# Performance work log

Hardware: AMD Instinct MI355X
Metric: run time of the kernel (lower is better)

The kernel has to match this reference:

```python
import jax, jax.numpy as jnp
import numpy as np

NU, NV = 8192, 8192
IN_DIM, HID, NCLS = 128, 64, 5


def setup_inputs() -> dict:
    key = jax.random.key(0)
    k1, k2, k3, k4, k5, k6, k7 = jax.random.split(key, 7)
    return {
        "u": jax.random.normal(k1, (NU, IN_DIM), dtype=jnp.float32),
        "v": jax.random.normal(k2, (NV, IN_DIM), dtype=jnp.float32),
        "adj": jax.random.uniform(k3, (NU, NV), dtype=jnp.float32),
        "degree": jax.random.uniform(k4, (NU + NV,), dtype=jnp.float32),
        "u_weight": jax.random.normal(k5, (NCLS, IN_DIM, HID), dtype=jnp.float32),
        "v_weight": jax.random.normal(k6, (NCLS, IN_DIM, HID), dtype=jnp.float32),
        "bias": jax.random.normal(k7, (HID,), dtype=jnp.float32),
        "r": 4,
    }


def reference(u, v, adj, degree, u_weight, v_weight, bias, r):
    # Sum weight slices for rating classes 0..r (r is a static Python int).
    Wu = jnp.sum(u_weight[: r + 1], axis=0)  # [IN_DIM, HID]
    Wv = jnp.sum(v_weight[: r + 1], axis=0)
    # Dropout is identity at p=0.0 (eval mode).
    su = u @ Wu  # [NU, HID]
    sv = v @ Wv  # [NV, HID]
    nu = adj.shape[0]
    # Block adjacency [[0, A], [A^T, 0]] row-scaled by diag(degree), applied to
    # concat(su, sv) -- computed block-wise, same math without the dense block matrix.
    top = degree[:nu, None] * (adj @ sv)      # [NU, HID]
    bot = degree[nu:, None] * (adj.T @ su)    # [NV, HID]
    return jnp.concatenate([top, bot], axis=0) + bias
```

## Files before the change

kernel.cpp:

```cpp
#include <hip/hip_runtime.h>
#include <stdint.h>


#define HID 64
#define IN_DIM 128
#define NROWS 8192
#define NCLS 5

typedef float f32x4 __attribute__((ext_vector_type(4)));
typedef short s16x8 __attribute__((ext_vector_type(8)));
typedef unsigned short u16;

static __device__ __forceinline__ short f2b(float x) {
    unsigned u = __builtin_bit_cast(unsigned, x);
    return (short)((u + 0x7FFFu + ((u >> 16) & 1u)) >> 16);
}

static __device__ __forceinline__ void cp16(const void* g, void* l) {
    __builtin_amdgcn_global_load_lds(
        (const __attribute__((address_space(1))) void*)g,
        (__attribute__((address_space(3))) void*)l, 16, 0, 0);
}

__global__ __launch_bounds__(256, 2) void k_prep(
    const float* __restrict__ u, const float* __restrict__ v,
    const float* __restrict__ uw, const float* __restrict__ vw,
    const int* __restrict__ rp, u16* __restrict__ ws)
{
    __shared__ float W[IN_DIM * HID];
    __shared__ float X[64 * 129];

    const int y = blockIdx.y;
    const float* __restrict__ src  = y ? v  : u;
    const float* __restrict__ wsrc = y ? vw : uw;
    u16* __restrict__ dstT = ws + (size_t)y * (HID * NROWS);
    const int i0 = blockIdx.x * 64;
    const int t = threadIdx.x;
    int r = *rp; if (r > NCLS - 1) r = NCLS - 1; if (r < 0) r = 0;

    for (int idx = t; idx < IN_DIM * HID; idx += 256) {
        float s = 0.f;
        for (int c = 0; c <= r; ++c) s += wsrc[c * (IN_DIM * HID) + idx];
        W[idx] = s;
    }
    #pragma unroll
    for (int qq = 0; qq < 8; ++qq) {
        int idx = t + qq * 256;
        int row = idx >> 5, c4 = idx & 31;
        f32x4 val = *(const f32x4*)&src[(size_t)(i0 + row) * IN_DIM + c4 * 4];
        float* d = &X[row * 129 + c4 * 4];
        d[0] = val[0]; d[1] = val[1]; d[2] = val[2]; d[3] = val[3];
    }
    __syncthreads();

    const int i = t & 63, h0 = (t >> 6) * 16;
    float acc[16];
    #pragma unroll
    for (int k = 0; k < 16; ++k) acc[k] = 0.f;
    for (int c = 0; c < IN_DIM; ++c) {
        float uv = X[i * 129 + c];
        const f32x4* wr = (const f32x4*)&W[c * HID + h0];
        f32x4 w0 = wr[0], w1 = wr[1], w2 = wr[2], w3 = wr[3];
        acc[0]  += uv * w0[0]; acc[1]  += uv * w0[1];
        acc[2]  += uv * w0[2]; acc[3]  += uv * w0[3];
        acc[4]  += uv * w1[0]; acc[5]  += uv * w1[1];
        acc[6]  += uv * w1[2]; acc[7]  += uv * w1[3];
        acc[8]  += uv * w2[0]; acc[9]  += uv * w2[1];
        acc[10] += uv * w2[2]; acc[11] += uv * w2[3];
        acc[12] += uv * w3[0]; acc[13] += uv * w3[1];
        acc[14] += uv * w3[2]; acc[15] += uv * w3[3];
    }
    #pragma unroll
    for (int hh = 0; hh < 16; ++hh)
        dstT[(size_t)(h0 + hh) * NROWS + i0 + i] = (u16)f2b(acc[hh]);
}

__global__ __launch_bounds__(256, 2) void k_main(
    const float* __restrict__ adj, const float* __restrict__ degree,
    const float* __restrict__ bias, const u16* __restrict__ ws,
    float* __restrict__ out)
{
    __shared__ float At[2][2048];
    __shared__ u16   Bt[2][4096];

    const int mode = blockIdx.y;
    const int bx = blockIdx.x;
    const int t = threadIdx.x;
    const int w = t >> 6, l = t & 63;
    const int q = l >> 4, l15 = l & 15;
    const int mt = w & 1;
    const int nh = w >> 1;
    const int m0 = bx * 32;
    const u16* __restrict__ BT = ws + (mode == 0 ? (size_t)(HID * NROWS) : 0);

    f32x4 acc[2];
    acc[0] = (f32x4){0.f, 0.f, 0.f, 0.f};
    acc[1] = (f32x4){0.f, 0.f, 0.f, 0.f};

    auto stage = [&](int step, int buf) {
        int kc = (mode == 0) ? (((bx >> 1) + step) & 127)
                             : (((bx >> 1) - step) & 127);
        int k0 = kc * 64;
        if (mode == 0) {
            #pragma unroll
            for (int t2 = 0; t2 < 2; ++t2) {
                int s = w * 2 + t2;
                int row = s * 4 + (l >> 4);
                int cg = (l & 15) ^ (row & 15);
                cp16(&adj[(size_t)(m0 + row) * NROWS + k0 + cg * 4],
                     &At[buf][s * 256]);
            }
        } else {
            #pragma unroll
            for (int t2 = 0; t2 < 2; ++t2) {
                int s = w * 2 + t2;
                int row = s * 8 + (l >> 3);
                int cg = (l & 7) ^ (row & 7);
                cp16(&adj[(size_t)(k0 + row) * NROWS + m0 + cg * 4],
                     &At[buf][s * 256]);
            }
        }
        #pragma unroll
        for (int t2 = 0; t2 < 2; ++t2) {
            int s = w * 2 + t2;
            int n = s * 8 + (l >> 3);
            int cg = (l & 7) ^ (n & 7);
            cp16(&BT[(size_t)n * NROWS + k0 + cg * 8], &Bt[buf][s * 512]);
        }
    };

    stage(0, 0);
    __syncthreads();
    int buf = 0;
    for (int step = 0; step < 128; ++step) {
        if (step < 127) stage(step + 1, buf ^ 1);
        const float* __restrict__ A = At[buf];
        const u16* __restrict__ B = Bt[buf];
        #pragma unroll
        for (int kh = 0; kh < 2; ++kh) {
            s16x8 af;
            if (mode == 0) {
                const int ii = mt * 16 + l15;
                const int cgk = kh * 8 + q * 2;
                f32x4 f0 = *(const f32x4*)&A[ii * 64 + ((cgk    ) ^ (ii & 15)) * 4];
                f32x4 f1 = *(const f32x4*)&A[ii * 64 + ((cgk + 1) ^ (ii & 15)) * 4];
                af[0] = f2b(f0[0]); af[1] = f2b(f0[1]);
                af[2] = f2b(f0[2]); af[3] = f2b(f0[3]);
                af[4] = f2b(f1[0]); af[5] = f2b(f1[1]);
                af[6] = f2b(f1[2]); af[7] = f2b(f1[3]);
            } else {
                const int jj = mt * 16 + l15;
                const int cg = jj >> 2, jr = jj & 3;
                #pragma unroll
                for (int tt = 0; tt < 8; ++tt) {
                    int ii = kh * 32 + q * 8 + tt;
                    af[tt] = f2b(A[ii * 32 + ((cg ^ (ii & 7)) << 2) + jr]);
                }
            }
            #pragma unroll
            for (int nn = 0; nn < 2; ++nn) {
                int n = (nh * 2 + nn) * 16 + l15;
                int cgl = (kh * 4 + q) ^ (n & 7);
                s16x8 bf = *(const s16x8*)&B[n * 64 + cgl * 8];
                acc[nn] = __builtin_amdgcn_mfma_f32_16x16x32_bf16(af, bf, acc[nn], 0, 0, 0);
            }
        }
        __syncthreads();
        buf ^= 1;
    }

    const int obase = (mode == 0) ? 0 : NROWS;
    const float* __restrict__ degp = degree + obase;
    #pragma unroll
    for (int nn = 0; nn < 2; ++nn) {
        int n = (nh * 2 + nn) * 16 + l15;
        float bs = bias[n];
        #pragma unroll
        for (int rg = 0; rg < 4; ++rg) {
            int m = m0 + mt * 16 + q * 4 + rg;
            out[(size_t)(obase + m) * HID + n] = degp[m] * acc[nn][rg] + bs;
        }
    }
}

extern "C" void kernel_launch(void* const* d_in, const int* in_sizes, int n_in,
                              void* d_out, int out_size, void* d_ws, size_t ws_size,
                              hipStream_t stream) {
    (void)in_sizes; (void)n_in; (void)out_size; (void)ws_size;
    const float* u      = (const float*)d_in[0];
    const float* v      = (const float*)d_in[1];
    const float* adj    = (const float*)d_in[2];
    const float* degree = (const float*)d_in[3];
    const float* uw     = (const float*)d_in[4];
    const float* vw     = (const float*)d_in[5];
    const float* bias   = (const float*)d_in[6];
    const int*   rp     = (const int*)d_in[7];
    u16*   ws  = (u16*)d_ws;
    float* out = (float*)d_out;

    k_prep<<<dim3(128, 2), 256, 0, stream>>>(u, v, uw, vw, rp, ws);
    k_main<<<dim3(256, 2), 256, 0, stream>>>(adj, degree, bias, ws, out);
}
```

Baseline: 493.3 us.

## Split K across waves with direct global loads and LDS reduction

Restructures k_main so each of the four waves owns a quarter of the K range and computes the full 32x64 output tile, rather than splitting the M/N tile across waves. The block-shared double-buffered global_load_lds staging and per-step __syncthreads are dropped. Mode 0 now loads adj and B fragments straight from global memory into registers. Mode 1 transposes through a per-wave padded LDS tile, and the four partial accumulators are summed in LDS at the end before vectorized stores. This removes block-wide barriers and lets waves run independently, at the cost of more registers, less sharing of B loads between waves, and uncoalesced direct global fragment loads.

```diff
diff --git a/kernel.cpp b/kernel.cpp
--- a/kernel.cpp
+++ b/kernel.cpp
@@ -14,12 +14,6 @@
 static __device__ __forceinline__ short f2b(float x) {
     unsigned u = __builtin_bit_cast(unsigned, x);
     return (short)((u + 0x7FFFu + ((u >> 16) & 1u)) >> 16);
-}
-
-static __device__ __forceinline__ void cp16(const void* g, void* l) {
-    __builtin_amdgcn_global_load_lds(
-        (const __attribute__((address_space(1))) void*)g,
-        (__attribute__((address_space(3))) void*)l, 16, 0, 0);
 }
 
 __global__ __launch_bounds__(256, 2) void k_prep(
@@ -80,107 +74,123 @@
     const float* __restrict__ bias, const u16* __restrict__ ws,
     float* __restrict__ out)
 {
-    __shared__ float At[2][2048];
-    __shared__ u16   Bt[2][4096];
+    __shared__ float S[4][64 * 33];
 
     const int mode = blockIdx.y;
     const int bx = blockIdx.x;
     const int t = threadIdx.x;
     const int w = t >> 6, l = t & 63;
     const int q = l >> 4, l15 = l & 15;
-    const int mt = w & 1;
-    const int nh = w >> 1;
     const int m0 = bx * 32;
+    const unsigned a = (unsigned)(bx >> 1);
+    const int kbase = w * 2048;
     const u16* __restrict__ BT = ws + (mode == 0 ? (size_t)(HID * NROWS) : 0);
 
-    f32x4 acc[2];
-    acc[0] = (f32x4){0.f, 0.f, 0.f, 0.f};
-    acc[1] = (f32x4){0.f, 0.f, 0.f, 0.f};
-
-    auto stage = [&](int step, int buf) {
-        int kc = (mode == 0) ? (((bx >> 1) + step) & 127)
-                             : (((bx >> 1) - step) & 127);
-        int k0 = kc * 64;
-        if (mode == 0) {
-            #pragma unroll
-            for (int t2 = 0; t2 < 2; ++t2) {
-                int s = w * 2 + t2;
-                int row = s * 4 + (l >> 4);
-                int cg = (l & 15) ^ (row & 15);
-                cp16(&adj[(size_t)(m0 + row) * NROWS + k0 + cg * 4],
-                     &At[buf][s * 256]);
-            }
-        } else {
-            #pragma unroll
-            for (int t2 = 0; t2 < 2; ++t2) {
-                int s = w * 2 + t2;
-                int row = s * 8 + (l >> 3);
-                int cg = (l & 7) ^ (row & 7);
-                cp16(&adj[(size_t)(k0 + row) * NROWS + m0 + cg * 4],
-                     &At[buf][s * 256]);
+    f32x4 acc[2][4];
+    #pragma unroll
+    for (int i = 0; i < 2; ++i)
+        #pragma unroll
+        for (int j = 0; j < 4; ++j) acc[i][j] = (f32x4){0.f, 0.f, 0.f, 0.f};
+
+    if (mode == 0) {
+        const float* __restrict__ ap0 = adj + (size_t)(m0 + l15) * NROWS;
+        const float* __restrict__ ap1 = ap0 + (size_t)16 * NROWS;
+        for (int tau = 0; tau < 32; ++tau) {
+            const int k0 = kbase + (int)(((a + tau) & 31u) << 6);
+            #pragma unroll
+            for (int kh = 0; kh < 2; ++kh) {
+                const int k = k0 + kh * 32 + q * 8;
+                f32x4 a00 = *(const f32x4*)(ap0 + k);
+                f32x4 a01 = *(const f32x4*)(ap0 + k + 4);
+                f32x4 a10 = *(const f32x4*)(ap1 + k);
+                f32x4 a11 = *(const f32x4*)(ap1 + k + 4);
+                s16x8 bf[4];
+                #pragma unroll
+                for (int nn = 0; nn < 4; ++nn)
+                    bf[nn] = *(const s16x8*)(BT + (size_t)(nn * 16 + l15) * NROWS + k);
+                s16x8 af0, af1;
+                af0[0]=f2b(a00[0]); af0[1]=f2b(a00[1]); af0[2]=f2b(a00[2]); af0[3]=f2b(a00[3]);
+                af0[4]=f2b(a01[0]); af0[5]=f2b(a01[1]); af0[6]=f2b(a01[2]); af0[7]=f2b(a01[3]);
+                af1[0]=f2b(a10[0]); af1[1]=f2b(a10[1]); af1[2]=f2b(a10[2]); af1[3]=f2b(a10[3]);
+                af1[4]=f2b(a11[0]); af1[5]=f2b(a11[1]); af1[6]=f2b(a11[2]); af1[7]=f2b(a11[3]);
+                #pragma unroll
+                for (int nn = 0; nn < 4; ++nn) {
+                    acc[0][nn] = __builtin_amdgcn_mfma_f32_16x16x32_bf16(af0, bf[nn], acc[0][nn], 0, 0, 0);
+                    acc[1][nn] = __builtin_amdgcn_mfma_f32_16x16x32_bf16(af1, bf[nn], acc[1][nn], 0, 0, 0);
+                }
             }
         }
-        #pragma unroll
-        for (int t2 = 0; t2 < 2; ++t2) {
-            int s = w * 2 + t2;
-            int n = s * 8 + (l >> 3);
-            int cg = (l & 7) ^ (n & 7);
-            cp16(&BT[(size_t)n * NROWS + k0 + cg * 8], &Bt[buf][s * 512]);
-        }
-    };
-
-    stage(0, 0);
-    __syncthreads();
-    int buf = 0;
-    for (int step = 0; step < 128; ++step) {
-        if (step < 127) stage(step + 1, buf ^ 1);
-        const float* __restrict__ A = At[buf];
-        const u16* __restrict__ B = Bt[buf];
-        #pragma unroll
-        for (int kh = 0; kh < 2; ++kh) {
-            s16x8 af;
-            if (mode == 0) {
-                const int ii = mt * 16 + l15;
-                const int cgk = kh * 8 + q * 2;
-                f32x4 f0 = *(const f32x4*)&A[ii * 64 + ((cgk    ) ^ (ii & 15)) * 4];
-                f32x4 f1 = *(const f32x4*)&A[ii * 64 + ((cgk + 1) ^ (ii & 15)) * 4];
-                af[0] = f2b(f0[0]); af[1] = f2b(f0[1]);
-                af[2] = f2b(f0[2]); af[3] = f2b(f0[3]);
-                af[4] = f2b(f1[0]); af[5] = f2b(f1[1]);
-                af[6] = f2b(f1[2]); af[7] = f2b(f1[3]);
-            } else {
-                const int jj = mt * 16 + l15;
-                const int cg = jj >> 2, jr = jj & 3;
-                #pragma unroll
-                for (int tt = 0; tt < 8; ++tt) {
-                    int ii = kh * 32 + q * 8 + tt;
-                    af[tt] = f2b(A[ii * 32 + ((cg ^ (ii & 7)) << 2) + jr]);
+    } else {
+        float* __restrict__ T = S[w];
+        const int wr_r = l >> 3;
+        const int wr_c = (l & 7) * 4;
+        const float* __restrict__ cb = adj + m0 + wr_c;
+        for (int tau = 0; tau < 32; ++tau) {
+            const int i0 = kbase + (int)(((a - tau) & 31u) << 6);
+            f32x4 tr[8];
+            #pragma unroll
+            for (int c = 0; c < 8; ++c)
+                tr[c] = *(const f32x4*)(cb + (size_t)(i0 + c * 8 + wr_r) * NROWS);
+            #pragma unroll
+            for (int c = 0; c < 8; ++c) {
+                float* d = &T[(c * 8 + wr_r) * 33 + wr_c];
+                d[0] = tr[c][0]; d[1] = tr[c][1]; d[2] = tr[c][2]; d[3] = tr[c][3];
+            }
+            asm volatile("s_waitcnt lgkmcnt(0)" ::: "memory");
+            #pragma unroll
+            for (int kh = 0; kh < 2; ++kh) {
+                const int kk = i0 + kh * 32 + q * 8;
+                s16x8 bf[4];
+                #pragma unroll
+                for (int nn = 0; nn < 4; ++nn)
+                    bf[nn] = *(const s16x8*)(BT + (size_t)(nn * 16 + l15) * NROWS + kk);
+                s16x8 af[2];
+                #pragma unroll
+                for (int mt = 0; mt < 2; ++mt) {
+                    const int j = mt * 16 + l15;
+                    #pragma unroll
+                    for (int tt = 0; tt < 8; ++tt)
+                        af[mt][tt] = f2b(T[(kh * 32 + q * 8 + tt) * 33 + j]);
+                }
+                #pragma unroll
+                for (int nn = 0; nn < 4; ++nn) {
+                    acc[0][nn] = __builtin_amdgcn_mfma_f32_16x16x32_bf16(af[0], bf[nn], acc[0][nn], 0, 0, 0);
+                    acc[1][nn] = __builtin_amdgcn_mfma_f32_16x16x32_bf16(af[1], bf[nn], acc[1][nn], 0, 0, 0);
                 }
             }
-            #pragma unroll
-            for (int nn = 0; nn < 2; ++nn) {
-                int n = (nh * 2 + nn) * 16 + l15;
-                int cgl = (kh * 4 + q) ^ (n & 7);
-                s16x8 bf = *(const s16x8*)&B[n * 64 + cgl * 8];
-                acc[nn] = __builtin_amdgcn_mfma_f32_16x16x32_bf16(af, bf, acc[nn], 0, 0, 0);
-            }
+            asm volatile("" ::: "memory");
         }
-        __syncthreads();
-        buf ^= 1;
-    }
-
-    const int obase = (mode == 0) ? 0 : NROWS;
-    const float* __restrict__ degp = degree + obase;
-    #pragma unroll
-    for (int nn = 0; nn < 2; ++nn) {
-        int n = (nh * 2 + nn) * 16 + l15;
-        float bs = bias[n];
+    }
+
+    asm volatile("" ::: "memory");
+    {
+        float* __restrict__ P = S[w];
         #pragma unroll
-        for (int rg = 0; rg < 4; ++rg) {
-            int m = m0 + mt * 16 + q * 4 + rg;
-            out[(size_t)(obase + m) * HID + n] = degp[m] * acc[nn][rg] + bs;
-        }
-    }
+        for (int mt = 0; mt < 2; ++mt)
+            #pragma unroll
+            for (int nn = 0; nn < 4; ++nn)
+                #pragma unroll
+                for (int rg = 0; rg < 4; ++rg)
+                    P[(mt * 16 + q * 4 + rg) * 64 + nn * 16 + l15] = acc[mt][nn][rg];
+    }
+    __syncthreads();
+
+    const int e0 = t * 8;
+    const int m = e0 >> 6, n = e0 & 63;
+    f32x4 s0 = (f32x4){0.f,0.f,0.f,0.f}, s1 = s0;
+    #pragma unroll
+    for (int ww = 0; ww < 4; ++ww) {
+        s0 += *(const f32x4*)&S[ww][e0];
+        s1 += *(const f32x4*)&S[ww][e0 + 4];
+    }
+    const int grow = (mode ? NROWS : 0) + m0 + m;
+    const float d = degree[grow];
+    f32x4 b0 = *(const f32x4*)&bias[n];
+    f32x4 b1 = *(const f32x4*)&bias[n + 4];
+    f32x4 o0 = d * s0 + b0;
+    f32x4 o1 = d * s1 + b1;
+    *(f32x4*)&out[(size_t)grow * HID + n]     = o0;
+    *(f32x4*)&out[(size_t)grow * HID + n + 4] = o1;
 }
 
 extern "C" void kernel_launch(void* const* d_in, const int* in_sizes, int n_in,
```

After: 482.0 us. 1.02x faster.
